# Kernel optimization log

Measured on AMD Instinct MI355X. Metric: run time of the kernel, lower is better.

The kernel has to match this reference:

```python
import jax, jax.numpy as jnp
import numpy as np

NEAR = 0.01
FAR = 10.0
MAX_ITERS = 32
N_RAYS = 65536
HIDDEN = 128


def setup_inputs() -> dict:
    key = jax.random.key(0)
    ks = jax.random.split(key, 12)
    f = jnp.float32
    origins = jax.random.normal(ks[0], (N_RAYS, 3), f) * 2.0
    directions = jax.random.normal(ks[1], (N_RAYS, 3), f)
    directions = directions / jnp.linalg.norm(directions, axis=-1, keepdims=True)
    s1 = 1.0 / np.sqrt(3.0)
    s2 = 1.0 / np.sqrt(HIDDEN)
    return {
        "origins": origins,
        "directions": directions,
        "W1": jax.random.normal(ks[2], (3, HIDDEN), f) * s1,
        "b1": jax.random.normal(ks[3], (HIDDEN,), f) * 0.01,
        "W2": jax.random.normal(ks[4], (HIDDEN, HIDDEN), f) * s2,
        "b2": jax.random.normal(ks[5], (HIDDEN,), f) * 0.01,
        "W3": jax.random.normal(ks[6], (HIDDEN, 1), f) * s2,
        "b3": jax.random.normal(ks[7], (1,), f) * 0.01,
        "Wc1": jax.random.normal(ks[8], (3, HIDDEN), f) * s1,
        "bc1": jax.random.normal(ks[9], (HIDDEN,), f) * 0.01,
        "Wc2": jax.random.normal(ks[10], (HIDDEN, 3), f) * s2,
        "bc2": jax.random.normal(ks[11], (3,), f) * 0.01,
    }


def reference(origins, directions, W1, b1, W2, b2, W3, b3, Wc1, bc1, Wc2, bc2):
    N = origins.shape[0]

    def sdf(p):  # [N,3] -> [N,1]
        h = jax.nn.relu(p @ W1 + b1)
        h = jax.nn.relu(h @ W2 + b2)
        return h @ W3 + b3

    def get_color(p):  # [N,3] -> [N,3]
        h = jax.nn.relu(p @ Wc1 + bc1)
        return jax.nn.sigmoid(h @ Wc2 + bc2)

    def step(state, _):
        points, distances, final_mask = state
        sdfs = sdf(points)                                  # [N,1]
        valid = (sdfs <= NEAR) & (distances < FAR)          # [N,1] bool
        final_mask = final_mask | valid
        upd = ~valid                                        # rays still marching
        distances = distances + jnp.where(upd, sdfs, 0.0)
        points = points + jnp.where(upd, directions * sdfs, 0.0)
        return (points, distances, final_mask), None

    init = (origins,
            jnp.zeros((N, 1), origins.dtype),
            jnp.zeros((N, 1), dtype=bool))
    (points, distances, final_mask), _ = jax.lax.scan(step, init, None, length=MAX_ITERS)
    final_mask = final_mask | (distances < FAR)             # [N,1]

    # color[mask] = get_color(points[mask]) <=> masked where (get_color is pointwise)
    color = jnp.where(final_mask, get_color(points), 0.0)   # [N,3]
    return color
```

## Files before the change

### kernel.cpp

```cpp
#include <hip/hip_runtime.h>

#define HIDDEN 128
#define N_RAYS 65536
#define NEAR_D 0.01f
#define FAR_D 10.0f
#define MAX_ITERS 32

typedef _Float16 f16x8 __attribute__((ext_vector_type(8)));
typedef float f32x16 __attribute__((ext_vector_type(16)));

__global__ void w2_frag_kernel(const float* __restrict__ W2,
                               _Float16* __restrict__ img) {
    int tid = blockIdx.x * blockDim.x + threadIdx.x;
    int j = tid & 7;
    int L = (tid >> 3) & 63;
    int tc = tid >> 9;
    int t = tc >> 3, c = tc & 7;
    int n = t * 32 + (L & 31);
    int k = c * 16 + ((L >> 5) & 1) * 8 + j;
    float w = W2[k * HIDDEN + n];
    _Float16 hi = (_Float16)w;
    _Float16 lo = (_Float16)(w - (float)hi);
    img[tid] = hi;
    img[16384 + tid] = lo;
}

__launch_bounds__(256, 2)
__global__ void sphere_trace_kernel(
    const float* __restrict__ origins,
    const float* __restrict__ directions,
    const float* __restrict__ W1,
    const float* __restrict__ b1,
    const _Float16* __restrict__ w2img,
    const float* __restrict__ b2,
    const float* __restrict__ W3,
    const float* __restrict__ b3,
    const float* __restrict__ Wc1,
    const float* __restrict__ bc1,
    const float* __restrict__ Wc2,
    const float* __restrict__ bc2,
    float* __restrict__ out)
{
    __shared__ __align__(16) _Float16 wlds[32768];
    __shared__ float sbuf[4][32];

    const int tid = threadIdx.x;
    const int lane = tid & 63;
    const int w = __builtin_amdgcn_readfirstlane(tid >> 6);
    const int q = lane >> 5;
    const int n32 = lane & 31;

    {
        const float4* src = (const float4*)w2img;
        float4* dst = (float4*)wlds;
        #pragma unroll
        for (int i = 0; i < 16; ++i)
            dst[tid + 256 * i] = src[tid + 256 * i];
    }
    __syncthreads();

    float bAx, bAy, bAz, bB;
    {
        bAx = fmaxf(fabsf(W1[lane]),              fabsf(W1[lane + 64]));
        bAy = fmaxf(fabsf(W1[HIDDEN + lane]),     fabsf(W1[HIDDEN + lane + 64]));
        bAz = fmaxf(fabsf(W1[2 * HIDDEN + lane]), fabsf(W1[2 * HIDDEN + lane + 64]));
        bB  = fmaxf(fabsf(b1[lane]),              fabsf(b1[lane + 64]));
        #pragma unroll
        for (int m = 1; m < 64; m <<= 1) {
            bAx = fmaxf(bAx, __shfl_xor(bAx, m));
            bAy = fmaxf(bAy, __shfl_xor(bAy, m));
            bAz = fmaxf(bAz, __shfl_xor(bAz, m));
            bB  = fmaxf(bB,  __shfl_xor(bB,  m));
        }
    }

    const int ray = blockIdx.x * 128 + w * 32 + n32;
    float px = 0.f, py = 0.f, pz = 0.f, dx = 0.f, dy = 0.f, dz = 0.f;
    float dist = 0.0f;
    bool frozen = true;
    if (lane < 32) {
        px = origins[ray * 3 + 0];
        py = origins[ray * 3 + 1];
        pz = origins[ray * 3 + 2];
        dx = directions[ray * 3 + 0];
        dy = directions[ray * 3 + 1];
        dz = directions[ray * 3 + 2];
        frozen = false;
    }

    float b2v[4], w3v[4];
    #pragma unroll
    for (int t = 0; t < 4; ++t) {
        b2v[t] = b2[t * 32 + n32];
        w3v[t] = W3[t * 32 + n32];
    }
    const float b3v = b3[0];
    const int q8 = q * 8;

    #pragma unroll 1
    for (int it = 0; it < MAX_ITERS; ++it) {
        const float ppx = __shfl(px, n32);
        const float ppy = __shfl(py, n32);
        const float ppz = __shfl(pz, n32);

        const float bound = fmaf(fabsf(ppx), bAx, fmaf(fabsf(ppy), bAy,
                            fmaf(fabsf(ppz), bAz, bB)));
        float sc = 1.0f, inv = 1.0f;
        {
            const int e = (int)((__float_as_uint(bound) >> 23) & 255u);
            if (e > 137) {
                const int sh = e - 137;
                sc  = __uint_as_float((unsigned)(127 - sh) << 23);
                inv = __uint_as_float((unsigned)(127 + sh) << 23);
            }
        }

        f32x16 acc[4];
        #pragma unroll
        for (int t = 0; t < 4; ++t)
            #pragma unroll
            for (int r = 0; r < 16; ++r) acc[t][r] = 0.0f;

        #pragma unroll 1
        for (int c = 0; c < 8; ++c) {
            f16x8 Ah, Al;
            {
                const int kb = c * 16 + q8;
                const float* wpx = W1 + kb;
                const float* wpy = W1 + HIDDEN + kb;
                const float* wpz = W1 + 2 * HIDDEN + kb;
                const float* bp  = b1 + kb;
                #pragma unroll
                for (int jj = 0; jj < 8; ++jj) {
                    const float hv = fmaxf(
                        fmaf(ppx, wpx[jj], fmaf(ppy, wpy[jj],
                        fmaf(ppz, wpz[jj], bp[jj]))), 0.0f);
                    const float x = hv * sc;
                    const _Float16 hi = (_Float16)x;
                    Ah[jj] = hi;
                    Al[jj] = (_Float16)(x - (float)hi);
                }
            }
            #pragma unroll
            for (int t = 0; t < 4; ++t) {
                const int off = ((t * 8 + c) << 9) + (lane << 3);
                const f16x8 bh = *(const f16x8*)(wlds + off);
                const f16x8 bl = *(const f16x8*)(wlds + 16384 + off);
                acc[t] = __builtin_amdgcn_mfma_f32_32x32x16_f16(Ah, bh, acc[t], 0, 0, 0);
                acc[t] = __builtin_amdgcn_mfma_f32_32x32x16_f16(Ah, bl, acc[t], 0, 0, 0);
                acc[t] = __builtin_amdgcn_mfma_f32_32x32x16_f16(Al, bh, acc[t], 0, 0, 0);
            }
        }

        float invr[16];
        #pragma unroll
        for (int r = 0; r < 16; ++r) {
            const int msrc = (r & 3) + 8 * (r >> 2) + 4 * q;
            invr[r] = __shfl(inv, msrc);
        }
        float ps[16];
        #pragma unroll
        for (int r = 0; r < 16; ++r) ps[r] = 0.0f;
        #pragma unroll
        for (int t = 0; t < 4; ++t) {
            #pragma unroll
            for (int r = 0; r < 16; ++r) {
                const float v = fmaxf(fmaf(acc[t][r], invr[r], b2v[t]), 0.0f);
                ps[r] = fmaf(v, w3v[t], ps[r]);
            }
        }

        #pragma unroll
        for (int mask = 1; mask < 32; mask <<= 1)
            #pragma unroll
            for (int r = 0; r < 16; ++r)
                ps[r] += __shfl_xor(ps[r], mask);
        if ((lane & 31) == 0) {
            #pragma unroll
            for (int r = 0; r < 16; ++r)
                sbuf[w][(r & 3) + 8 * (r >> 2) + 4 * q] = ps[r];
        }
        float s = 0.0f;
        if (lane < 32) s = sbuf[w][lane] + b3v;

        if (lane < 32) {
            const bool valid = (s <= NEAR_D) && (dist < FAR_D);
            if (!frozen) {
                if (valid) {
                    frozen = true;
                } else {
                    dist += s;
                    px = fmaf(dx, s, px);
                    py = fmaf(dy, s, py);
                    pz = fmaf(dz, s, pz);
                }
            }
        }
        if (__ballot((lane < 32) && !frozen) == 0) break;
    }

    const int k0 = lane, k1 = lane + 64;
    const float cx0 = Wc1[k0], cx1 = Wc1[k1];
    const float cy0 = Wc1[HIDDEN + k0], cy1 = Wc1[HIDDEN + k1];
    const float cz0 = Wc1[2 * HIDDEN + k0], cz1 = Wc1[2 * HIDDEN + k1];
    const float cb0 = bc1[k0], cb1 = bc1[k1];
    const float u00 = Wc2[k0 * 3 + 0], u01 = Wc2[k0 * 3 + 1], u02 = Wc2[k0 * 3 + 2];
    const float u10 = Wc2[k1 * 3 + 0], u11 = Wc2[k1 * 3 + 1], u12 = Wc2[k1 * 3 + 2];

    float g0 = 0.f, g1 = 0.f, g2 = 0.f;
    #pragma unroll 1
    for (int m = 0; m < 32; ++m) {
        const float qx = __shfl(px, m);
        const float qy = __shfl(py, m);
        const float qz = __shfl(pz, m);
        const float h0 = fmaxf(fmaf(qx, cx0, fmaf(qy, cy0, fmaf(qz, cz0, cb0))), 0.f);
        const float h1 = fmaxf(fmaf(qx, cx1, fmaf(qy, cy1, fmaf(qz, cz1, cb1))), 0.f);
        float a0 = fmaf(h0, u00, h1 * u10);
        float a1 = fmaf(h0, u01, h1 * u11);
        float a2 = fmaf(h0, u02, h1 * u12);
        #pragma unroll
        for (int mask = 1; mask < 64; mask <<= 1) {
            a0 += __shfl_xor(a0, mask);
            a1 += __shfl_xor(a1, mask);
            a2 += __shfl_xor(a2, mask);
        }
        if (lane == m) { g0 = a0; g1 = a1; g2 = a2; }
    }

    if (lane < 32) {
        float c0 = 0.f, c1 = 0.f, c2 = 0.f;
        if (frozen || dist < FAR_D) {
            c0 = 1.0f / (1.0f + __expf(-(g0 + bc2[0])));
            c1 = 1.0f / (1.0f + __expf(-(g1 + bc2[1])));
            c2 = 1.0f / (1.0f + __expf(-(g2 + bc2[2])));
        }
        out[ray * 3 + 0] = c0;
        out[ray * 3 + 1] = c1;
        out[ray * 3 + 2] = c2;
    }
}

extern "C" void kernel_launch(void* const* d_in, const int* in_sizes, int n_in,
                              void* d_out, int out_size, void* d_ws, size_t ws_size,
                              hipStream_t stream) {
    const float* origins    = (const float*)d_in[0];
    const float* directions = (const float*)d_in[1];
    const float* W1  = (const float*)d_in[2];
    const float* b1  = (const float*)d_in[3];
    const float* W2  = (const float*)d_in[4];
    const float* b2  = (const float*)d_in[5];
    const float* W3  = (const float*)d_in[6];
    const float* b3  = (const float*)d_in[7];
    const float* Wc1 = (const float*)d_in[8];
    const float* bc1 = (const float*)d_in[9];
    const float* Wc2 = (const float*)d_in[10];
    const float* bc2 = (const float*)d_in[11];
    float* out = (float*)d_out;

    _Float16* w2img = (_Float16*)d_ws;

    w2_frag_kernel<<<64, 256, 0, stream>>>(W2, w2img);

    sphere_trace_kernel<<<N_RAYS / 128, 256, 0, stream>>>(
        origins, directions, W1, b1, w2img, b2, W3, b3,
        Wc1, bc1, Wc2, bc2, out);
}
```

Before: 315.5 us.

## Cache first W2 tile in registers, unroll K loop, use DPP half-wave reductions

Preloads the W2 fragments for the first output tile into registers so each iteration issues fewer LDS reads, and fully unrolls the 8-step K loop. Replaces the shfl_xor butterfly reduction over 32 lanes with a DPP row-shift/row-bcast prefix sum, so the total lands in lane 31 of each half-wave and is written to shared memory with vectorized float4 stores. This cuts LDS and cross-lane shuffle traffic. The extra 64 VGPRs of cached weights and the full unroll raise register pressure and could hurt occupancy under launch_bounds(256,2).

```diff
diff --git a/kernel.cpp b/kernel.cpp
--- a/kernel.cpp
+++ b/kernel.cpp
@@ -8,6 +8,20 @@
 
 typedef _Float16 f16x8 __attribute__((ext_vector_type(8)));
 typedef float f32x16 __attribute__((ext_vector_type(16)));
+
+template <int CTRL, int ROW_MASK>
+__device__ __forceinline__ float dpp_add(float v) {
+    int s = __builtin_amdgcn_update_dpp(0, __float_as_int(v), CTRL, ROW_MASK, 0xF, true);
+    return v + __int_as_float(s);
+}
+__device__ __forceinline__ float half_sum_dpp(float v) {
+    v = dpp_add<0x111, 0xF>(v);
+    v = dpp_add<0x112, 0xF>(v);
+    v = dpp_add<0x114, 0xF>(v);
+    v = dpp_add<0x118, 0xF>(v);
+    v = dpp_add<0x142, 0xA>(v);
+    return v;
+}
 
 __global__ void w2_frag_kernel(const float* __restrict__ W2,
                                _Float16* __restrict__ img) {
@@ -59,6 +73,13 @@
     }
     __syncthreads();
 
+    f16x8 B0h[8], B0l[8];
+    #pragma unroll
+    for (int c = 0; c < 8; ++c) {
+        B0h[c] = *(const f16x8*)(wlds + (c << 9) + (lane << 3));
+        B0l[c] = *(const f16x8*)(wlds + 16384 + (c << 9) + (lane << 3));
+    }
+
     float bAx, bAy, bAz, bB;
     {
         bAx = fmaxf(fabsf(W1[lane]),              fabsf(W1[lane + 64]));
@@ -121,7 +142,7 @@
             #pragma unroll
             for (int r = 0; r < 16; ++r) acc[t][r] = 0.0f;
 
-        #pragma unroll 1
+        #pragma unroll
         for (int c = 0; c < 8; ++c) {
             f16x8 Ah, Al;
             {
@@ -141,8 +162,11 @@
                     Al[jj] = (_Float16)(x - (float)hi);
                 }
             }
-            #pragma unroll
-            for (int t = 0; t < 4; ++t) {
+            acc[0] = __builtin_amdgcn_mfma_f32_32x32x16_f16(Ah, B0h[c], acc[0], 0, 0, 0);
+            acc[0] = __builtin_amdgcn_mfma_f32_32x32x16_f16(Ah, B0l[c], acc[0], 0, 0, 0);
+            acc[0] = __builtin_amdgcn_mfma_f32_32x32x16_f16(Al, B0h[c], acc[0], 0, 0, 0);
+            #pragma unroll
+            for (int t = 1; t < 4; ++t) {
                 const int off = ((t * 8 + c) << 9) + (lane << 3);
                 const f16x8 bh = *(const f16x8*)(wlds + off);
                 const f16x8 bl = *(const f16x8*)(wlds + 16384 + off);
@@ -171,14 +195,19 @@
         }
 
         #pragma unroll
-        for (int mask = 1; mask < 32; mask <<= 1)
-            #pragma unroll
-            for (int r = 0; r < 16; ++r)
-                ps[r] += __shfl_xor(ps[r], mask);
-        if ((lane & 31) == 0) {
-            #pragma unroll
-            for (int r = 0; r < 16; ++r)
-                sbuf[w][(r & 3) + 8 * (r >> 2) + 4 * q] = ps[r];
+        for (int r = 0; r < 16; ++r)
+            ps[r] = half_sum_dpp(ps[r]);
+        if ((lane & 31) == 31) {
+            const int mb = q * 4;
+            #pragma unroll
+            for (int g = 0; g < 4; ++g) {
+                float4 v4;
+                v4.x = ps[4 * g + 0];
+                v4.y = ps[4 * g + 1];
+                v4.z = ps[4 * g + 2];
+                v4.w = ps[4 * g + 3];
+                *(float4*)&sbuf[w][8 * g + mb] = v4;
+            }
         }
         float s = 0.0f;
         if (lane < 32) s = sbuf[w][lane] + b3v;
```

After: 1.214 ms. +284.7%, slower.
